# Kernel tuning notes

Hardware: AMD Instinct MI355X
Metric: run time of the kernel (lower is better)

The kernel has to match this reference:

```python
import jax, jax.numpy as jnp
import numpy as np

B, S, D, H = 2, 2048, 1024, 16
HS = D // H  # head_size = 64


def setup_inputs() -> dict:
    key = jax.random.key(0)
    k1, k2, k3 = jax.random.split(key, 3)
    x = jax.random.normal(k1, (B, S, D), dtype=jnp.float32)
    c_attn_w = jax.random.normal(k2, (D, 3 * D), dtype=jnp.float32) * (1.0 / np.sqrt(D))
    c_attn_b = jnp.zeros((3 * D,), dtype=jnp.float32)
    c_proj_w = jax.random.normal(k3, (D, D), dtype=jnp.float32) * (1.0 / np.sqrt(D))
    c_proj_b = jnp.zeros((D,), dtype=jnp.float32)
    return {"x": x, "c_attn_w": c_attn_w, "c_attn_b": c_attn_b,
            "c_proj_w": c_proj_w, "c_proj_b": c_proj_b}


def reference(x, c_attn_w, c_attn_b, c_proj_w, c_proj_b):
    b, s, d = x.shape
    qkv = x @ c_attn_w + c_attn_b  # [b, s, 3d]
    q, k, v = jnp.split(qkv, 3, axis=-1)
    # [b, h, s, hs]
    q = q.reshape(b, s, H, HS).transpose(0, 2, 1, 3)
    k = k.reshape(b, s, H, HS).transpose(0, 2, 1, 3)
    v = v.reshape(b, s, H, HS).transpose(0, 2, 1, 3)
    scale = jnp.float32(HS) ** -0.5
    scores = jnp.einsum('bhqd,bhkd->bhqk', q, k) * scale  # [b, h, s, s]
    causal = jnp.tril(jnp.ones((s, s), dtype=bool))
    scores = jnp.where(causal[None, None, :, :], scores, jnp.float32(-jnp.inf))
    weights = jax.nn.softmax(scores, axis=-1)  # attn_dropout p=0 -> identity
    attn = jnp.einsum('bhqk,bhkd->bhqd', weights, v)  # [b, h, s, hs]
    attn = attn.transpose(0, 2, 1, 3).reshape(b, s, d)
    out = attn @ c_proj_w + c_proj_b  # resid_dropout p=0 -> identity
    return out
```

## Files before the change

### kernel.cpp

```cpp
#include <hip/hip_runtime.h>
#include <hip/hip_bf16.h>
#include <stdint.h>

#define TB 2
#define TS 2048
#define TD 1024
#define TH 16
#define THS 64
#define TK 1024

typedef __attribute__((ext_vector_type(8))) short short8;
typedef __attribute__((ext_vector_type(4))) short short4v;
typedef __attribute__((ext_vector_type(4))) float f32x4;
typedef __attribute__((ext_vector_type(16))) float f32x16;
typedef __attribute__((ext_vector_type(4))) unsigned int uint4v;

static __device__ __forceinline__ unsigned short f2bf(float f) {
  union { float f; unsigned u; } v; v.f = f;
  unsigned r = v.u + 0x7FFFu + ((v.u >> 16) & 1u);
  return (unsigned short)(r >> 16);
}

static __device__ __forceinline__ float bf2f(unsigned short u) {
  union { unsigned u; float f; } v; v.u = ((unsigned)u) << 16;
  return v.f;
}

static __device__ __forceinline__ unsigned cvtpk(float a, float b) {
  unsigned r;
  asm("v_cvt_pk_bf16_f32 %0, %1, %2" : "=v"(r) : "v"(a), "v"(b));
  return r;
}

static __device__ __forceinline__ void swap32(unsigned& a, unsigned& b) {
  asm("v_permlane32_swap_b32 %0, %1" : "+v"(a), "+v"(b));
}

static __device__ __forceinline__ void async_copy16(const void* g, void* l) {
  __builtin_amdgcn_global_load_lds(
      (const __attribute__((address_space(1))) unsigned int*)g,
      (__attribute__((address_space(3))) unsigned int*)l, 16, 0, 0);
}

__global__ __launch_bounds__(256) void k_cvt_bf16x4(const float* __restrict__ in,
                                                    ushort4* __restrict__ out, int n4) {
  int i = blockIdx.x * blockDim.x + threadIdx.x;
  if (i >= n4) return;
  float4 v = ((const float4*)in)[i];
  out[i] = make_ushort4(f2bf(v.x), f2bf(v.y), f2bf(v.z), f2bf(v.w));
}

__global__ __launch_bounds__(256) void k_transpose_bf(const float* __restrict__ in,
                                                      unsigned short* __restrict__ out,
                                                      int R, int C) {
  __shared__ float tile[32][33];
  const int tx = threadIdx.x & 31, ty = threadIdx.x >> 5;
  const int r0 = blockIdx.y * 32, c0 = blockIdx.x * 32;
#pragma unroll
  for (int i = 0; i < 32; i += 8)
    tile[ty + i][tx] = in[(size_t)(r0 + ty + i) * C + c0 + tx];
  __syncthreads();
#pragma unroll
  for (int i = 0; i < 32; i += 8)
    out[(size_t)(c0 + ty + i) * R + r0 + tx] = f2bf(tile[tx][ty + i]);
}

__device__ __forceinline__ void gemm_core_k1024(const unsigned short* __restrict__ A,
                                                const unsigned short* __restrict__ BT,
                                                int m0, int n0,
                                                unsigned short* sA, unsigned short* sB,
                                                f32x4 acc[4][4]) {
  const int tid = threadIdx.x;
  const int wave = tid >> 6, lane = tid & 63;
  const int wm = wave >> 1, wn = wave & 1;

  const unsigned short* gsrc = (wave < 2) ? A : BT;
  const int row0 = (wave < 2) ? m0 : n0;
  unsigned short* lbase = (wave < 2) ? sA : sB;
  const int cw = (wave & 1) * 4;
  const size_t gr = (size_t)(row0 + cw * 16 + (lane >> 2)) * TK + (lane & 3) * 8;

#pragma unroll
  for (int mi = 0; mi < 4; ++mi)
#pragma unroll
    for (int ni = 0; ni < 4; ++ni)
      acc[mi][ni] = (f32x4){0.f, 0.f, 0.f, 0.f};

  auto stage = [&](int buf, int kt) {
    const unsigned short* g = gsrc + gr + kt * 32;
    unsigned short* l = lbase + buf * 4096 + cw * 512;
#pragma unroll
    for (int c = 0; c < 4; ++c)
      async_copy16(g + (size_t)c * 16 * TK, l + c * 512);
  };

  stage(0, 0);
  __syncthreads();

  const int l15 = lane & 15, lk8 = (lane >> 4) * 8;
  const int aoff = (wm * 64 + l15) * 32 + lk8;
  const int boff = (wn * 64 + l15) * 32 + lk8;

  for (int kt = 0; kt < TK / 32; ++kt) {
    const int buf = kt & 1;
    if (kt + 1 < TK / 32) stage(buf ^ 1, kt + 1);
    short8 af[4], bfr[4];
#pragma unroll
    for (int i = 0; i < 4; ++i) {
      af[i] = *(const short8*)&sA[buf * 4096 + aoff + i * 16 * 32];
      bfr[i] = *(const short8*)&sB[buf * 4096 + boff + i * 16 * 32];
    }
#pragma unroll
    for (int mi = 0; mi < 4; ++mi)
#pragma unroll
      for (int ni = 0; ni < 4; ++ni)
        acc[mi][ni] = __builtin_amdgcn_mfma_f32_16x16x32_bf16(af[mi], bfr[ni], acc[mi][ni], 0, 0, 0);
    __syncthreads();
  }
}

__global__ __launch_bounds__(256) void k_gemm_qkv(const unsigned short* __restrict__ A,
                                                  const unsigned short* __restrict__ BT,
                                                  const float* __restrict__ bias,
                                                  unsigned short* __restrict__ Qo,
                                                  unsigned short* __restrict__ Ko,
                                                  unsigned short* __restrict__ VTo) {
  __shared__ unsigned short smem[4 * 64 * 68];
  unsigned short* sA = smem;
  unsigned short* sB = smem + 8192;
  f32x4 acc[4][4];
  const int m0 = blockIdx.y * 128, n0 = blockIdx.x * 128;
  gemm_core_k1024(A, BT, m0, n0, sA, sB, acc);

  const int lane = threadIdx.x & 63, wave = threadIdx.x >> 6;
  const int wm = wave >> 1, wn = wave & 1;
  const int lr4 = (lane >> 4) * 4, l15 = lane & 15;

  const int col0 = n0 + wn * 64;
  const int reg = col0 >> 10;
  const int h0 = (col0 & 1023) >> 6;
  const bool isV = (reg == 2);
  const int t0 = m0 + wm * 64;
  const int b = t0 >> 11;
  const int s0 = t0 & 2047;

  unsigned short* tw = smem + wave * (64 * 68);
#pragma unroll
  for (int mi = 0; mi < 4; ++mi) {
#pragma unroll
    for (int ni = 0; ni < 4; ++ni) {
      const int c = ni * 16 + l15;
      const float bi = bias[col0 + c];
#pragma unroll
      for (int j = 0; j < 4; ++j) {
        const int r = mi * 16 + lr4 + j;
        tw[isV ? (c * 68 + r) : (r * 68 + c)] = f2bf(acc[mi][ni][j] + bi);
      }
    }
  }
  unsigned short* outp;
  size_t rstride;
  if (isV) {
    outp = VTo + (((size_t)b * TH + h0) * THS) * TS + s0;
    rstride = TS;
  } else {
    outp = (reg == 0 ? Qo : Ko) + (((size_t)b * TH + h0) * TS + s0) * THS;
    rstride = THS;
  }
#pragma unroll
  for (int p2 = 0; p2 < 8; ++p2) {
    const int rp = p2 * 8 + (lane >> 3);
    const int co = (lane & 7) * 8;
    union { short4v h[2]; short8 s8; } u;
    u.h[0] = *(const short4v*)&tw[rp * 68 + co];
    u.h[1] = *(const short4v*)&tw[rp * 68 + co + 4];
    *(short8*)(outp + (size_t)rp * rstride + co) = u.s8;
  }
}

__global__ __launch_bounds__(256) void k_attn(const unsigned short* __restrict__ Q,
                                              const unsigned short* __restrict__ K,
                                              const unsigned short* __restrict__ VT,
                                              unsigned short* __restrict__ attn,
                                              unsigned short* __restrict__ pO,
                                              float2* __restrict__ pML) {
  __shared__ unsigned short sO[4][32 * 68];
  const int lane = threadIdx.x & 63, wave = threadIdx.x >> 6;
  const int l31 = lane & 31, h = lane >> 5;
  int c = blockIdx.x * 4 + wave;
  const int hh = blockIdx.y, b = blockIdx.z;
  if (b) c = 95 - c;

  int w, lo, hi, jhalf;
  if (c < 64) { w = c; lo = 0; hi = (w < 32) ? (w + 1) : 32; jhalf = 0; }
  else        { w = c - 32; lo = 32; hi = w + 1; jhalf = 1; }
  const bool partial = (w >= 32);
  const bool diag = (hi - 1 == w);
  const int qrb = w * 32;

  const unsigned short* Qh = Q + (((size_t)b * TH + hh) * TS) * THS;
  const unsigned short* Kh = K + (((size_t)b * TH + hh) * TS) * THS;
  const unsigned short* Vh = VT + (((size_t)b * TH + hh) * THS) * TS;

  short8 qf[4];
#pragma unroll
  for (int c2 = 0; c2 < 4; ++c2)
    qf[c2] = *(const short8*)&Qh[(size_t)(qrb + l31) * THS + c2 * 16 + h * 8];

  f32x16 o0 = {}, o1 = {};
  float m_run = -1e30f, l_run = 0.f;
  const float cl2e = 0.125f * 1.44269504088896340736f;
  const float THR = 8.0f / cl2e;

  short8 kf[4];
#pragma unroll
  for (int c2 = 0; c2 < 4; ++c2)
    kf[c2] = *(const short8*)&Kh[(size_t)(lo * 32 + l31) * THS + c2 * 16 + h * 8];

  for (int kt = lo; kt < hi; ++kt) {
    const int kb = kt * 32;
    short8 vf[2][2];
#pragma unroll
    for (int t = 0; t < 2; ++t)
#pragma unroll
      for (int c2 = 0; c2 < 2; ++c2)
        vf[t][c2] = *(const short8*)&Vh[(size_t)(t * 32 + l31) * TS + kb + c2 * 16 + h * 8];

    f32x16 s = {};
#pragma unroll
    for (int c2 = 0; c2 < 4; ++c2)
      s = __builtin_amdgcn_mfma_f32_32x32x16_bf16(kf[c2], qf[c2], s, 0, 0, 0);

    if (kt + 1 < hi) {
#pragma unroll
      for (int c2 = 0; c2 < 4; ++c2)
        kf[c2] = *(const short8*)&Kh[(size_t)(kb + 32 + l31) * THS + c2 * 16 + h * 8];
    }

    if (diag && kt == hi - 1) {
#pragma unroll
      for (int r = 0; r < 16; ++r)
        if ((r & 3) + 8 * (r >> 2) + 4 * h > l31) s[r] = -1e30f;
    }

    const float ma = fmaxf(fmaxf(s[0], s[1]), fmaxf(s[2], s[3]));
    const float mb = fmaxf(fmaxf(s[4], s[5]), fmaxf(s[6], s[7]));
    const float mc = fmaxf(fmaxf(s[8], s[9]), fmaxf(s[10], s[11]));
    const float md = fmaxf(fmaxf(s[12], s[13]), fmaxf(s[14], s[15]));
    float tm = fmaxf(fmaxf(ma, mb), fmaxf(mc, md));
    tm = fmaxf(tm, __shfl_xor(tm, 32));

    float al;
    if (__all(tm <= m_run + THR)) {
      al = 1.0f;
    } else {
      const float mn = fmaxf(m_run, tm);
      al = __builtin_amdgcn_exp2f((m_run - mn) * cl2e);
      m_run = mn;
      o0 *= al;
      o1 *= al;
    }
#pragma unroll
    for (int r = 0; r < 16; ++r)
      s[r] = __builtin_amdgcn_exp2f((s[r] - m_run) * cl2e);
    const float sa = (s[0] + s[1]) + (s[2] + s[3]);
    const float sb2 = (s[4] + s[5]) + (s[6] + s[7]);
    const float sc = (s[8] + s[9]) + (s[10] + s[11]);
    const float sd = (s[12] + s[13]) + (s[14] + s[15]);
    float ts = (sa + sb2) + (sc + sd);
    ts += __shfl_xor(ts, 32);
    l_run = l_run * al + ts;

    unsigned B0 = cvtpk(s[0], s[1]), B1 = cvtpk(s[2], s[3]);
    unsigned B2 = cvtpk(s[4], s[5]), B3 = cvtpk(s[6], s[7]);
    swap32(B0, B2);
    swap32(B1, B3);
    unsigned B4 = cvtpk(s[8], s[9]), B5 = cvtpk(s[10], s[11]);
    unsigned B6 = cvtpk(s[12], s[13]), B7 = cvtpk(s[14], s[15]);
    swap32(B4, B6);
    swap32(B5, B7);
    union U { uint4v u; short8 s8; } u0, u1;
    u0.u = (uint4v){B0, B1, B2, B3};
    u1.u = (uint4v){B4, B5, B6, B7};

    o0 = __builtin_amdgcn_mfma_f32_32x32x16_bf16(vf[0][0], u0.s8, o0, 0, 0, 0);
    o0 = __builtin_amdgcn_mfma_f32_32x32x16_bf16(vf[0][1], u1.s8, o0, 0, 0, 0);
    o1 = __builtin_amdgcn_mfma_f32_32x32x16_bf16(vf[1][0], u0.s8, o1, 0, 0, 0);
    o1 = __builtin_amdgcn_mfma_f32_32x32x16_bf16(vf[1][1], u1.s8, o1, 0, 0, 0);
  }

  const float inv = partial ? 1.0f : (1.0f / l_run);
  unsigned* so32 = (unsigned*)&sO[wave][0];
#pragma unroll
  for (int j2 = 0; j2 < 8; ++j2) {
    const int d0 = ((2 * j2) & 3) + 8 * (j2 >> 1) + 4 * h;
    so32[l31 * 34 + (d0 >> 1)] = cvtpk(o0[2 * j2] * inv, o0[2 * j2 + 1] * inv);
    so32[l31 * 34 + ((32 + d0) >> 1)] = cvtpk(o1[2 * j2] * inv, o1[2 * j2 + 1] * inv);
  }
  if (!partial) {
#pragma unroll
    for (int p2 = 0; p2 < 4; ++p2) {
      const int rp = p2 * 8 + (lane >> 3);
      const int co = (lane & 7) * 8;
      short4v va = *(const short4v*)&sO[wave][rp * 68 + co];
      short4v vb = *(const short4v*)&sO[wave][rp * 68 + co + 4];
      unsigned short* gp = &attn[(size_t)(b * TS + qrb + rp) * TD + hh * THS + co];
      *(short4v*)gp = va;
      *(short4v*)(gp + 4) = vb;
    }
  } else {
    const int p = ((b * TH + hh) * 32 + (w - 32)) * 2 + jhalf;
    unsigned short* gp0 = pO + (size_t)p * 32 * 64;
#pragma unroll
    for (int p2 = 0; p2 < 4; ++p2) {
      const int rp = p2 * 8 + (lane >> 3);
      const int co = (lane & 7) * 8;
      union { short4v h[2]; short8 s8; } u;
      u.h[0] = *(const short4v*)&sO[wave][rp * 68 + co];
      u.h[1] = *(const short4v*)&sO[wave][rp * 68 + co + 4];
      *(short8*)(gp0 + rp * 64 + co) = u.s8;
    }
    if (h == 0) pML[p * 32 + l31] = make_float2(m_run, l_run);
  }
}

__global__ __launch_bounds__(64) void k_attn_combine(const unsigned short* __restrict__ pO,
                                                     const float2* __restrict__ pML,
                                                     unsigned short* __restrict__ attn) {
  const int d = threadIdx.x;
  const int wx = blockIdx.x;
  const int hh = blockIdx.y, b = blockIdx.z;
  const int p = ((b * TH + hh) * 32 + wx) * 2;
  const float cl2e = 0.125f * 1.44269504088896340736f;
  const unsigned short* oa = pO + (size_t)p * 32 * 64;
  const unsigned short* ob = oa + 32 * 64;
#pragma unroll 4
  for (int r = 0; r < 32; ++r) {
    const float2 A = pML[p * 32 + r];
    const float2 Bv = pML[(p + 1) * 32 + r];
    const float m = fmaxf(A.x, Bv.x);
    const float eA = __builtin_amdgcn_exp2f((A.x - m) * cl2e);
    const float eB = __builtin_amdgcn_exp2f((Bv.x - m) * cl2e);
    const float linv = 1.0f / (A.y * eA + Bv.y * eB);
    const float o = (bf2f(oa[r * 64 + d]) * eA + bf2f(ob[r * 64 + d]) * eB) * linv;
    attn[(size_t)(b * TS + (32 + wx) * 32 + r) * TD + hh * THS + d] = f2bf(o);
  }
}

__global__ __launch_bounds__(256) void k_gemm_proj(const unsigned short* __restrict__ A,
                                                   const unsigned short* __restrict__ BT,
                                                   const float* __restrict__ bias,
                                                   float* __restrict__ out) {
  __shared__ unsigned short sA[2 * 4096];
  __shared__ unsigned short sB[2 * 4096];
  f32x4 acc[4][4];
  const int m0 = blockIdx.y * 128, n0 = blockIdx.x * 128;
  gemm_core_k1024(A, BT, m0, n0, sA, sB, acc);

  const int lane = threadIdx.x & 63, wave = threadIdx.x >> 6;
  const int wm = wave >> 1, wn = wave & 1;
  const int lr4 = (lane >> 4) * 4, l15 = lane & 15;
#pragma unroll
  for (int mi = 0; mi < 4; ++mi) {
    const int row = m0 + wm * 64 + mi * 16 + lr4;
#pragma unroll
    for (int ni = 0; ni < 4; ++ni) {
      const int col = n0 + wn * 64 + ni * 16 + l15;
      const float bi = bias[col];
#pragma unroll
      for (int j = 0; j < 4; ++j)
        out[(size_t)(row + j) * TD + col] = acc[mi][ni][j] + bi;
    }
  }
}

extern "C" void kernel_launch(void* const* d_in, const int* in_sizes, int n_in,
                              void* d_out, int out_size, void* d_ws, size_t ws_size,
                              hipStream_t stream) {
  const float* x = (const float*)d_in[0];
  const float* c_attn_w = (const float*)d_in[1];
  const float* c_attn_b = (const float*)d_in[2];
  const float* c_proj_w = (const float*)d_in[3];
  const float* c_proj_b = (const float*)d_in[4];
  float* out = (float*)d_out;

  const size_t SZ_XB = (size_t)4096 * 1024 * 2;
  const size_t SZ_WAT = (size_t)3072 * 1024 * 2;
  const size_t SZ_WPT = (size_t)1024 * 1024 * 2;
  const size_t SZ_HEAD = (size_t)TB * TH * TS * THS * 2;
  const size_t SZ_ATT = (size_t)4096 * 1024 * 2;
  if (ws_size < SZ_XB + SZ_WAT + SZ_WPT + 3 * SZ_HEAD + SZ_ATT) return;

  char* ws = (char*)d_ws;
  unsigned short* xb = (unsigned short*)ws;   ws += SZ_XB;
  unsigned short* waT = (unsigned short*)ws;  ws += SZ_WAT;
  unsigned short* wpT = (unsigned short*)ws;  ws += SZ_WPT;
  unsigned short* Qb = (unsigned short*)ws;   ws += SZ_HEAD;
  unsigned short* Kb = (unsigned short*)ws;   ws += SZ_HEAD;
  unsigned short* VTb = (unsigned short*)ws;  ws += SZ_HEAD;
  unsigned short* attn = (unsigned short*)ws; ws += SZ_ATT;

  unsigned short* pO = xb;
  float2* pML = (float2*)waT;

  k_cvt_bf16x4<<<4096, 256, 0, stream>>>(x, (ushort4*)xb, 4096 * 1024 / 4);
  k_transpose_bf<<<dim3(3072 / 32, 1024 / 32), 256, 0, stream>>>(c_attn_w, waT, 1024, 3072);
  k_transpose_bf<<<dim3(1024 / 32, 1024 / 32), 256, 0, stream>>>(c_proj_w, wpT, 1024, 1024);
  k_gemm_qkv<<<dim3(3072 / 128, 4096 / 128), 256, 0, stream>>>(xb, waT, c_attn_b, Qb, Kb, VTb);
  k_attn<<<dim3(24, TH, TB), 256, 0, stream>>>(Qb, Kb, VTb, attn, pO, pML);
  k_attn_combine<<<dim3(32, TH, TB), 64, 0, stream>>>(pO, pML, attn);
  k_gemm_proj<<<dim3(1024 / 128, 4096 / 128), 256, 0, stream>>>(attn, wpT, c_proj_b, out);
}
```

Before: 246.6 us.

## Split every causal query tile's KV range in half across waves with paired tiles

The attention kernel now gives each query tile two waves, each handling half of its causal key range. Tile j is paired with tile 63-j inside one block so every block does the same amount of work. Previously only the long tiles (w>=32) were split, and the work was balanced across 96 wave-tasks. Every tile now writes unnormalized partial outputs plus row max and sum, and the combine kernel merges all 64 tiles. This brings more waves and better balance, but adds combine work and extra global traffic for every tile.

```diff
diff --git a/kernel.cpp b/kernel.cpp
--- a/kernel.cpp
+++ b/kernel.cpp
@@ -187,16 +187,16 @@
   __shared__ unsigned short sO[4][32 * 68];
   const int lane = threadIdx.x & 63, wave = threadIdx.x >> 6;
   const int l31 = lane & 31, h = lane >> 5;
-  int c = blockIdx.x * 4 + wave;
+  const int j = blockIdx.x;
   const int hh = blockIdx.y, b = blockIdx.z;
-  if (b) c = 95 - c;
-
-  int w, lo, hi, jhalf;
-  if (c < 64) { w = c; lo = 0; hi = (w < 32) ? (w + 1) : 32; jhalf = 0; }
-  else        { w = c - 32; lo = 32; hi = w + 1; jhalf = 1; }
-  const bool partial = (w >= 32);
-  const bool diag = (hi - 1 == w);
-  const int qrb = w * 32;
+
+  const int wt = (wave < 2) ? j : 63 - j;
+  const int hw = (wt + 2) >> 1;
+  const int half1 = wave & 1;
+  const int lo = half1 ? hw : 0;
+  const int hi = half1 ? (wt + 1) : hw;
+  const bool diag = (hi == wt + 1) && (hi > lo);
+  const int qrb = wt * 32;
 
   const unsigned short* Qh = Q + (((size_t)b * TH + hh) * TS) * THS;
   const unsigned short* Kh = K + (((size_t)b * TH + hh) * TS) * THS;
@@ -289,28 +289,25 @@
     o1 = __builtin_amdgcn_mfma_f32_32x32x16_bf16(vf[1][1], u1.s8, o1, 0, 0, 0);
   }
 
-  const float inv = partial ? 1.0f : (1.0f / l_run);
   unsigned* so32 = (unsigned*)&sO[wave][0];
 #pragma unroll
   for (int j2 = 0; j2 < 8; ++j2) {
     const int d0 = ((2 * j2) & 3) + 8 * (j2 >> 1) + 4 * h;
-    so32[l31 * 34 + (d0 >> 1)] = cvtpk(o0[2 * j2] * inv, o0[2 * j2 + 1] * inv);
-    so32[l31 * 34 + ((32 + d0) >> 1)] = cvtpk(o1[2 * j2] * inv, o1[2 * j2 + 1] * inv);
-  }
-  if (!partial) {
+    so32[l31 * 34 + (d0 >> 1)] = cvtpk(o0[2 * j2], o0[2 * j2 + 1]);
+    so32[l31 * 34 + ((32 + d0) >> 1)] = cvtpk(o1[2 * j2], o1[2 * j2 + 1]);
+  }
+  if (!half1) {
 #pragma unroll
     for (int p2 = 0; p2 < 4; ++p2) {
       const int rp = p2 * 8 + (lane >> 3);
       const int co = (lane & 7) * 8;
-      short4v va = *(const short4v*)&sO[wave][rp * 68 + co];
-      short4v vb = *(const short4v*)&sO[wave][rp * 68 + co + 4];
-      unsigned short* gp = &attn[(size_t)(b * TS + qrb + rp) * TD + hh * THS + co];
-      *(short4v*)gp = va;
-      *(short4v*)(gp + 4) = vb;
+      union { short4v h[2]; short8 s8; } u;
+      u.h[0] = *(const short4v*)&sO[wave][rp * 68 + co];
+      u.h[1] = *(const short4v*)&sO[wave][rp * 68 + co + 4];
+      *(short8*)(&attn[(size_t)(b * TS + qrb + rp) * TD + hh * THS + co]) = u.s8;
     }
   } else {
-    const int p = ((b * TH + hh) * 32 + (w - 32)) * 2 + jhalf;
-    unsigned short* gp0 = pO + (size_t)p * 32 * 64;
+    unsigned short* gp0 = pO + ((size_t)((b * TH + hh) * 64 + wt)) * 32 * 64;
 #pragma unroll
     for (int p2 = 0; p2 < 4; ++p2) {
       const int rp = p2 * 8 + (lane >> 3);
@@ -320,30 +317,32 @@
       u.h[1] = *(const short4v*)&sO[wave][rp * 68 + co + 4];
       *(short8*)(gp0 + rp * 64 + co) = u.s8;
     }
-    if (h == 0) pML[p * 32 + l31] = make_float2(m_run, l_run);
-  }
+  }
+  if (h == 0)
+    pML[((size_t)((b * TH + hh) * 64 + wt) * 2 + half1) * 32 + l31] =
+        make_float2(m_run, l_run);
 }
 
 __global__ __launch_bounds__(64) void k_attn_combine(const unsigned short* __restrict__ pO,
                                                      const float2* __restrict__ pML,
                                                      unsigned short* __restrict__ attn) {
   const int d = threadIdx.x;
-  const int wx = blockIdx.x;
+  const int wt = blockIdx.x;
   const int hh = blockIdx.y, b = blockIdx.z;
-  const int p = ((b * TH + hh) * 32 + wx) * 2;
+  const int base = (b * TH + hh) * 64 + wt;
   const float cl2e = 0.125f * 1.44269504088896340736f;
-  const unsigned short* oa = pO + (size_t)p * 32 * 64;
-  const unsigned short* ob = oa + 32 * 64;
+  const unsigned short* ob = pO + (size_t)base * 32 * 64;
 #pragma unroll 4
   for (int r = 0; r < 32; ++r) {
-    const float2 A = pML[p * 32 + r];
-    const float2 Bv = pML[(p + 1) * 32 + r];
+    const float2 A = pML[((size_t)base * 2 + 0) * 32 + r];
+    const float2 Bv = pML[((size_t)base * 2 + 1) * 32 + r];
     const float m = fmaxf(A.x, Bv.x);
     const float eA = __builtin_amdgcn_exp2f((A.x - m) * cl2e);
     const float eB = __builtin_amdgcn_exp2f((Bv.x - m) * cl2e);
     const float linv = 1.0f / (A.y * eA + Bv.y * eB);
-    const float o = (bf2f(oa[r * 64 + d]) * eA + bf2f(ob[r * 64 + d]) * eB) * linv;
-    attn[(size_t)(b * TS + (32 + wx) * 32 + r) * TD + hh * THS + d] = f2bf(o);
+    const size_t ai = (size_t)(b * TS + wt * 32 + r) * TD + hh * THS + d;
+    const float o = (bf2f(attn[ai]) * eA + bf2f(ob[r * 64 + d]) * eB) * linv;
+    attn[ai] = f2bf(o);
   }
 }
 
@@ -407,7 +406,7 @@
   k_transpose_bf<<<dim3(3072 / 32, 1024 / 32), 256, 0, stream>>>(c_attn_w, waT, 1024, 3072);
   k_transpose_bf<<<dim3(1024 / 32, 1024 / 32), 256, 0, stream>>>(c_proj_w, wpT, 1024, 1024);
   k_gemm_qkv<<<dim3(3072 / 128, 4096 / 128), 256, 0, stream>>>(xb, waT, c_attn_b, Qb, Kb, VTb);
-  k_attn<<<dim3(24, TH, TB), 256, 0, stream>>>(Qb, Kb, VTb, attn, pO, pML);
-  k_attn_combine<<<dim3(32, TH, TB), 64, 0, stream>>>(pO, pML, attn);
+  k_attn<<<dim3(32, TH, TB), 256, 0, stream>>>(Qb, Kb, VTb, attn, pO, pML);
+  k_attn_combine<<<dim3(64, TH, TB), 64, 0, stream>>>(pO, pML, attn);
   k_gemm_proj<<<dim3(1024 / 128, 4096 / 128), 256, 0, stream>>>(attn, wpT, c_proj_b, out);
 }
```

Result: faster. 221.8 us (-10.0%).
